# Performance work log

Hardware: AMD Instinct MI355X
Metric: run time of the kernel (lower is better)

## Reference

```python
import jax, jax.numpy as jnp
import numpy as np

GROUP_SIZE = 32
FP8_MAX = 448.0
EPS = 1e-8


def fp8_pseudo_quantize_groupwise(x):
    """Per-group (contiguous groups of GROUP_SIZE along last dim) fp8-e4m3
    pseudo-quantization: scale to fp8 range, cast to fp8, cast back, rescale."""
    shape = x.shape
    g = shape[-1] // GROUP_SIZE
    xg = x.reshape(*shape[:-1], g, GROUP_SIZE)
    amax = jnp.max(jnp.abs(xg), axis=-1, keepdims=True)
    scale = jnp.maximum(amax, EPS) / FP8_MAX  # fp32 per-group scale
    q = (xg / scale).astype(jnp.float8_e4m3fn).astype(x.dtype)
    return (q * scale).reshape(shape)


def setup_inputs() -> dict:
    key = jax.random.key(0)
    k1, k2, k3 = jax.random.split(key, 3)
    B, S, K, N = 4, 2048, 4096, 4096
    x = jax.random.normal(k1, (B, S, K), dtype=jnp.float32)
    # Linear-like init scale for weight/bias
    W = jax.random.normal(k2, (N, K), dtype=jnp.float32) * (1.0 / np.sqrt(K))
    bias = jax.random.normal(k3, (N,), dtype=jnp.float32) * (1.0 / np.sqrt(K))
    return {"x": x, "W": W, "bias": bias}


def reference(x, W, bias):
    # pseudo mode, a_bit=8 < 16: quantize both activations and weight
    Wq = fp8_pseudo_quantize_groupwise(W)   # [N, K]
    xq = fp8_pseudo_quantize_groupwise(x)   # [B, S, K]
    # F.linear: xq @ Wq.T + bias
    out = jnp.einsum('bsk,nk->bsn', xq, Wq) + bias
    return out
```

## Files before the change

### kernel.cpp

```cpp
#include <hip/hip_runtime.h>
#include <hip/hip_bf16.h>

typedef __bf16 bf16x8 __attribute__((ext_vector_type(8)));
typedef float floatx4 __attribute__((ext_vector_type(4)));
typedef unsigned short ushortx8 __attribute__((ext_vector_type(8)));

#define FP8_MAX 448.0f
#define QEPS 1e-8f

#define GLLDS16(gptr, lptr)                                                          \
  __builtin_amdgcn_global_load_lds((const __attribute__((address_space(1))) void*)(gptr), \
                                   (__attribute__((address_space(3))) void*)(lptr), 16, 0, 0)

__global__ __launch_bounds__(256) void quant_dq_kernel(
    const float* __restrict__ src, __hip_bfloat16* __restrict__ dst, long long n)
{
    long long t = (long long)blockIdx.x * blockDim.x + threadIdx.x;
    long long base = t * 8;
    if (base >= n) return;

    const float4 v0 = *(const float4*)(src + base);
    const float4 v1 = *(const float4*)(src + base + 4);

    float am = fmaxf(
        fmaxf(fmaxf(fabsf(v0.x), fabsf(v0.y)), fmaxf(fabsf(v0.z), fabsf(v0.w))),
        fmaxf(fmaxf(fabsf(v1.x), fabsf(v1.y)), fmaxf(fabsf(v1.z), fabsf(v1.w))));
    am = fmaxf(am, __shfl_xor(am, 1));
    am = fmaxf(am, __shfl_xor(am, 2));
    const float scale = fmaxf(am, QEPS) / FP8_MAX;

    int p0 = __builtin_amdgcn_cvt_pk_fp8_f32(v0.x / scale, v0.y / scale, 0, false);
    int p1 = __builtin_amdgcn_cvt_pk_fp8_f32(v0.z / scale, v0.w / scale, 0, false);
    int p2 = __builtin_amdgcn_cvt_pk_fp8_f32(v1.x / scale, v1.y / scale, 0, false);
    int p3 = __builtin_amdgcn_cvt_pk_fp8_f32(v1.z / scale, v1.w / scale, 0, false);

    float r0 = __builtin_amdgcn_cvt_f32_fp8(p0, 0) * scale;
    float r1 = __builtin_amdgcn_cvt_f32_fp8(p0, 1) * scale;
    float r2 = __builtin_amdgcn_cvt_f32_fp8(p1, 0) * scale;
    float r3 = __builtin_amdgcn_cvt_f32_fp8(p1, 1) * scale;
    float r4 = __builtin_amdgcn_cvt_f32_fp8(p2, 0) * scale;
    float r5 = __builtin_amdgcn_cvt_f32_fp8(p2, 1) * scale;
    float r6 = __builtin_amdgcn_cvt_f32_fp8(p3, 0) * scale;
    float r7 = __builtin_amdgcn_cvt_f32_fp8(p3, 1) * scale;

    alignas(16) __hip_bfloat16 hb[8] = {
        __float2bfloat16(r0), __float2bfloat16(r1),
        __float2bfloat16(r2), __float2bfloat16(r3),
        __float2bfloat16(r4), __float2bfloat16(r5),
        __float2bfloat16(r6), __float2bfloat16(r7)};
    *(ushortx8*)(dst + base) = *(const ushortx8*)hb;
}


#define BAR() __builtin_amdgcn_s_barrier()
#define LGKM0()                                              \
  do {                                                       \
    asm volatile("s_waitcnt lgkmcnt(0)" ::: "memory");       \
    __builtin_amdgcn_sched_barrier(0);                       \
  } while (0)
#define VMCNT(n) asm volatile("s_waitcnt vmcnt(" #n ")" ::: "memory")

#define STAGE_A(a_, t_, b_)                                                   \
  do {                                                                        \
    const __hip_bfloat16* g_ = gAs + (long)(a_) * 128 * K + (long)(t_) * 64;  \
    __hip_bfloat16* l_ = &sA[(b_)][(a_) * 8192 + tid * 8];                    \
    GLLDS16(g_, l_);                                                          \
    GLLDS16(g_ + 64 * (long)K, l_ + 4096);                                    \
  } while (0)

#define STAGE_B(a_, t_, b_)                                                   \
  do {                                                                        \
    const __hip_bfloat16* g_ = gBs + (long)(a_) * 128 * K + (long)(t_) * 64;  \
    __hip_bfloat16* l_ = &sB[(b_)][(a_) * 8192 + tid * 8];                    \
    GLLDS16(g_, l_);                                                          \
    GLLDS16(g_ + 64 * (long)K, l_ + 4096);                                    \
  } while (0)

#define LOAD_A(buf, mh)                                                       \
  do {                                                                        \
    _Pragma("unroll") for (int mm = 0; mm < 4; ++mm)                          \
    _Pragma("unroll") for (int ks = 0; ks < 2; ++ks)                          \
        af[mm][ks] = *(const bf16x8*)((buf) + ((mh)*4 + mm) * 1024 + aoff[ks]); \
  } while (0)

#define LOAD_B(buf, nh)                                                       \
  do {                                                                        \
    _Pragma("unroll") for (int nn = 0; nn < 2; ++nn)                          \
    _Pragma("unroll") for (int ks = 0; ks < 2; ++ks)                          \
        bfr[nh][nn][ks] = *(const bf16x8*)((buf) + (nh)*2048 + nn * 1024 + boff[ks]); \
  } while (0)

#define QUAD(mh, nh)                                                          \
  do {                                                                        \
    __builtin_amdgcn_s_setprio(1);                                            \
    _Pragma("unroll") for (int ks = 0; ks < 2; ++ks)                          \
    _Pragma("unroll") for (int mm = 0; mm < 4; ++mm)                          \
    _Pragma("unroll") for (int nn = 0; nn < 2; ++nn)                          \
        acc[(mh)*4 + mm][(nh)*2 + nn] = __builtin_amdgcn_mfma_f32_16x16x32_bf16( \
            af[mm][ks], bfr[nh][nn][ks], acc[(mh)*4 + mm][(nh)*2 + nn], 0, 0, 0); \
    __builtin_amdgcn_s_setprio(0);                                            \
  } while (0)

__global__ __launch_bounds__(512, 2) void gemm_bias_kernel(
    const __hip_bfloat16* __restrict__ A,
    const __hip_bfloat16* __restrict__ B,
    const float* __restrict__ bias,
    float* __restrict__ C,
    int M, int N, int K)
{
    __shared__ __attribute__((aligned(16))) __hip_bfloat16 sA[2][256 * 64];
    __shared__ __attribute__((aligned(16))) __hip_bfloat16 sB[2][256 * 64];

    const int tid  = threadIdx.x;
    const int lane = tid & 63;
    const int wave = tid >> 6;
    const int wm   = wave >> 2;
    const int wn   = wave & 3;

    const int nwg = gridDim.x;
    const int wg  = blockIdx.x;
    int swz = wg;
    if ((nwg & 7) == 0) swz = (wg & 7) * (nwg >> 3) + (wg >> 3);
    const int NXB = N >> 8;
    const long bm = (long)(swz / NXB) * 256;
    const long bn = (long)(swz % NXB) * 256;

    const int srow   = tid >> 3;
    const int schunk = (tid & 7) ^ (srow & 7);
    const __hip_bfloat16* gAs = A + (bm + srow) * (long)K + schunk * 8;
    const __hip_bfloat16* gBs = B + (bn + srow) * (long)K + schunk * 8;

    const int fr = lane & 15;
    const int fq = lane >> 4;
    const int f7 = fr & 7;
    int aoff[2], boff[2];
#pragma unroll
    for (int ks = 0; ks < 2; ++ks) {
        const int ch = ((ks * 4 + fq) ^ f7) * 8;
        aoff[ks] = (wm * 128 + fr) * 64 + ch;
        boff[ks] = (wn * 64 + fr) * 64 + ch;
    }

    floatx4 acc[8][4];
#pragma unroll
    for (int i = 0; i < 8; ++i)
#pragma unroll
        for (int j = 0; j < 4; ++j)
            acc[i][j] = (floatx4){0.f, 0.f, 0.f, 0.f};

    bf16x8 af[4][2];
    bf16x8 bfr[2][2][2];

    const int NT = K >> 6;
    const int NI = NT >> 1;

    STAGE_A(0, 0, 0); STAGE_A(1, 0, 0);
    STAGE_B(0, 0, 0); STAGE_B(1, 0, 0);
    if (NT > 1) { STAGE_B(0, 1, 1); STAGE_B(1, 1, 1); STAGE_A(0, 1, 1); }
    VMCNT(6);
    BAR();

#pragma unroll 1
    for (int i = 0; i < NI; ++i) {
        const bool more = (i + 1 < NI);
        const int t1 = 2 * i + 1, t2 = 2 * i + 2, t3 = 2 * i + 3;

        LOAD_A(sA[0], 0); LOAD_B(sB[0], 0);
        STAGE_A(1, t1, 1);
        BAR(); LGKM0();
        QUAD(0, 0);
        BAR();

        LOAD_B(sB[0], 1);
        BAR(); LGKM0();
        QUAD(0, 1);
        BAR();

        LOAD_A(sA[0], 1);
        if (more) STAGE_B(0, t2, 0);
        BAR(); LGKM0();
        QUAD(1, 0);
        BAR();

        if (more) { STAGE_B(1, t2, 0); STAGE_A(0, t2, 0); }
        BAR();
        QUAD(1, 1);
        if (more) { VMCNT(6); } else { VMCNT(0); }
        BAR();

        LOAD_A(sA[1], 0); LOAD_B(sB[1], 0);
        if (more) STAGE_A(1, t2, 0);
        BAR(); LGKM0();
        QUAD(0, 0);
        BAR();

        LOAD_B(sB[1], 1);
        BAR(); LGKM0();
        QUAD(0, 1);
        BAR();

        LOAD_A(sA[1], 1);
        if (more) STAGE_B(0, t3, 1);
        BAR(); LGKM0();
        QUAD(1, 0);
        BAR();

        if (more) { STAGE_B(1, t3, 1); STAGE_A(0, t3, 1); }
        BAR();
        QUAD(1, 1);
        if (more) { VMCNT(6); }
        BAR();
    }

    const int rq = (lane >> 4) * 4;
#pragma unroll
    for (int j = 0; j < 4; ++j) {
        const long gc = bn + wn * 64 + j * 16 + fr;
        const float bj = bias[gc];
#pragma unroll
        for (int mf = 0; mf < 8; ++mf) {
            const long gr = bm + wm * 128 + mf * 16 + rq;
            float* cp = C + gr * (long)N + gc;
#pragma unroll
            for (int r = 0; r < 4; ++r)
                cp[(long)r * N] = acc[mf][j][r] + bj;
        }
    }
}

extern "C" void kernel_launch(void* const* d_in, const int* in_sizes, int n_in,
                              void* d_out, int out_size, void* d_ws, size_t ws_size,
                              hipStream_t stream) {
    const float* x    = (const float*)d_in[0];
    const float* W    = (const float*)d_in[1];
    const float* bias = (const float*)d_in[2];
    float* out = (float*)d_out;

    const long long nx = in_sizes[0];
    const long long nw = in_sizes[1];
    const int N = in_sizes[2];
    const int K = (int)(nw / N);
    const int M = (int)(nx / K);

    __hip_bfloat16* xq = (__hip_bfloat16*)d_ws;
    __hip_bfloat16* wq = xq + nx;

    {
        long long tx = nx / 8;
        int blocks = (int)((tx + 255) / 256);
        quant_dq_kernel<<<blocks, 256, 0, stream>>>(x, xq, nx);
    }
    {
        long long tw = nw / 8;
        int blocks = (int)((tw + 255) / 256);
        quant_dq_kernel<<<blocks, 256, 0, stream>>>(W, wq, nw);
    }

    dim3 grid((N / 256) * (M / 256));
    gemm_bias_kernel<<<grid, 512, 0, stream>>>(xq, wq, bias, out, M, N, K);
}
```

Measured before the change: 532.2 us.

## Replace fine-grained 8-phase GEMM pipeline with simple whole-tile double buffering

Replaces the interleaved per-quadrant staging schedule, with its many barriers and explicit lgkmcnt waits, with a plain double-buffered loop. Each half-iteration issues the next full tile's global-to-LDS loads, computes on the current buffer, then waits for all loads and syncs once. This removes most barriers and the manual LDS wait/sched-barrier fences. In exchange, load issue becomes burstier, the compiler now schedules the LDS reads itself, and there is no longer a finer-grained overlap of staging with MFMA work.

```diff
diff --git a/kernel.cpp b/kernel.cpp
--- a/kernel.cpp
+++ b/kernel.cpp
@@ -53,11 +53,6 @@
 
 
 #define BAR() __builtin_amdgcn_s_barrier()
-#define LGKM0()                                              \
-  do {                                                       \
-    asm volatile("s_waitcnt lgkmcnt(0)" ::: "memory");       \
-    __builtin_amdgcn_sched_barrier(0);                       \
-  } while (0)
 #define VMCNT(n) asm volatile("s_waitcnt vmcnt(" #n ")" ::: "memory")
 
 #define STAGE_A(a_, t_, b_)                                                   \
@@ -74,6 +69,12 @@
     __hip_bfloat16* l_ = &sB[(b_)][(a_) * 8192 + tid * 8];                    \
     GLLDS16(g_, l_);                                                          \
     GLLDS16(g_ + 64 * (long)K, l_ + 4096);                                    \
+  } while (0)
+
+#define STAGE_TILE(t_, b_)                                                    \
+  do {                                                                        \
+    STAGE_A(0, t_, b_); STAGE_A(1, t_, b_);                                   \
+    STAGE_B(0, t_, b_); STAGE_B(1, t_, b_);                                   \
   } while (0)
 
 #define LOAD_A(buf, mh)                                                       \
@@ -99,6 +100,17 @@
         acc[(mh)*4 + mm][(nh)*2 + nn] = __builtin_amdgcn_mfma_f32_16x16x32_bf16( \
             af[mm][ks], bfr[nh][nn][ks], acc[(mh)*4 + mm][(nh)*2 + nn], 0, 0, 0); \
     __builtin_amdgcn_s_setprio(0);                                            \
+  } while (0)
+
+#define COMPUTE(bufA, bufB)                                                   \
+  do {                                                                        \
+    LOAD_A(bufA, 0); LOAD_B(bufB, 0);                                         \
+    QUAD(0, 0);                                                               \
+    LOAD_B(bufB, 1);                                                          \
+    QUAD(0, 1);                                                               \
+    LOAD_A(bufA, 1);                                                          \
+    QUAD(1, 0);                                                               \
+    QUAD(1, 1);                                                               \
   } while (0)
 
 __global__ __launch_bounds__(512, 2) void gemm_bias_kernel(
@@ -154,61 +166,20 @@
     const int NT = K >> 6;
     const int NI = NT >> 1;
 
-    STAGE_A(0, 0, 0); STAGE_A(1, 0, 0);
-    STAGE_B(0, 0, 0); STAGE_B(1, 0, 0);
-    if (NT > 1) { STAGE_B(0, 1, 1); STAGE_B(1, 1, 1); STAGE_A(0, 1, 1); }
-    VMCNT(6);
+    STAGE_TILE(0, 0);
+    VMCNT(0);
     BAR();
 
 #pragma unroll 1
     for (int i = 0; i < NI; ++i) {
-        const bool more = (i + 1 < NI);
-        const int t1 = 2 * i + 1, t2 = 2 * i + 2, t3 = 2 * i + 3;
-
-        LOAD_A(sA[0], 0); LOAD_B(sB[0], 0);
-        STAGE_A(1, t1, 1);
-        BAR(); LGKM0();
-        QUAD(0, 0);
+        STAGE_TILE(2 * i + 1, 1);
+        COMPUTE(sA[0], sB[0]);
+        VMCNT(0);
         BAR();
 
-        LOAD_B(sB[0], 1);
-        BAR(); LGKM0();
-        QUAD(0, 1);
-        BAR();
-
-        LOAD_A(sA[0], 1);
-        if (more) STAGE_B(0, t2, 0);
-        BAR(); LGKM0();
-        QUAD(1, 0);
-        BAR();
-
-        if (more) { STAGE_B(1, t2, 0); STAGE_A(0, t2, 0); }
-        BAR();
-        QUAD(1, 1);
-        if (more) { VMCNT(6); } else { VMCNT(0); }
-        BAR();
-
-        LOAD_A(sA[1], 0); LOAD_B(sB[1], 0);
-        if (more) STAGE_A(1, t2, 0);
-        BAR(); LGKM0();
-        QUAD(0, 0);
-        BAR();
-
-        LOAD_B(sB[1], 1);
-        BAR(); LGKM0();
-        QUAD(0, 1);
-        BAR();
-
-        LOAD_A(sA[1], 1);
-        if (more) STAGE_B(0, t3, 1);
-        BAR(); LGKM0();
-        QUAD(1, 0);
-        BAR();
-
-        if (more) { STAGE_B(1, t3, 1); STAGE_A(0, t3, 1); }
-        BAR();
-        QUAD(1, 1);
-        if (more) { VMCNT(6); }
+        if (i + 1 < NI) STAGE_TILE(2 * i + 2, 0);
+        COMPUTE(sA[1], sB[1]);
+        VMCNT(0);
         BAR();
     }
 
```

New measurement: 536.1 us. No clear change (+0.7%).
